# Kernel optimization log

Hardware: AMD Instinct MI355X
Metric: run time of the kernel (lower is better)

The kernel has to match this reference:

```python
import jax, jax.numpy as jnp
import numpy as np

H, D = 8, 16          # heads, per-head dim (hidden=128)
N_NEWS, N_INTER, F_IN, C_OUT = 30000, 60000, 768, 4
HID = H * D


def setup_inputs() -> dict:
    key = jax.random.key(0)
    ks = jax.random.split(key, 20)
    s = lambda i, shape, sc=0.05: (jax.random.normal(ks[i], shape, dtype=jnp.float32) * sc)
    inp = {
        "x_news": jax.random.normal(ks[0], (N_NEWS, F_IN), dtype=jnp.float32),
        "x_inter": jax.random.normal(ks[1], (N_INTER, F_IN), dtype=jnp.float32),
        "edge_nn": jax.random.randint(ks[2], (2, 480000), 0, N_NEWS),
        "edge_in": jax.random.randint(ks[3], (2, 960000), 0, N_NEWS),
        # per-node-type input projections (HANConv.proj)
        "W_news": s(4, (F_IN, HID)), "b_news": jnp.zeros((HID,), jnp.float32),
        "W_inter": s(5, (F_IN, HID)), "b_inter": jnp.zeros((HID,), jnp.float32),
        # per-edge-type node-level attention vectors (lin_src / lin_dst)
        "a_src_nn": s(6, (H, D), 0.2), "a_dst_nn": s(7, (H, D), 0.2),
        "a_src_in": s(8, (H, D), 0.2), "a_dst_in": s(9, (H, D), 0.2),
        # semantic-level attention (k_lin, q)
        "Wk": s(10, (HID, HID)), "bk": jnp.zeros((HID,), jnp.float32),
        "q": s(11, (HID,), 0.2),
        # output head
        "W_out": s(12, (HID, C_OUT)), "b_out": jnp.zeros((C_OUT,), jnp.float32),
    }
    return inp


def _han_conv(h_src, h_dst, edge, a_src, a_dst, n_dst):
    # node-level (GAT-style) attention for one edge type
    asrc = (h_src * a_src).sum(-1)            # [Ns, H]
    adst = (h_dst * a_dst).sum(-1)            # [Nd, H]
    src, dst = edge[0], edge[1]
    e = jax.nn.leaky_relu(asrc[src] + adst[dst], negative_slope=0.2)   # [E, H]
    m = jax.ops.segment_max(e, dst, num_segments=n_dst)                # [Nd, H]
    m = jnp.where(jnp.isfinite(m), m, jnp.float32(0))
    ex = jnp.exp(e - m[dst])
    denom = jax.ops.segment_sum(ex, dst, num_segments=n_dst)
    alpha = ex / (denom[dst] + jnp.float32(1e-16))                     # [E, H]
    out = jax.ops.segment_sum(h_src[src] * alpha[:, :, None], dst, num_segments=n_dst)
    return jax.nn.relu(out.reshape(n_dst, H * D))                      # [Nd, HID]


def reference(x_news, x_inter, edge_nn, edge_in,
              W_news, b_news, W_inter, b_inter,
              a_src_nn, a_dst_nn, a_src_in, a_dst_in,
              Wk, bk, q, W_out, b_out):
    # per-node-type projection, reshape to heads
    h_news = (x_news @ W_news + b_news).reshape(-1, H, D)
    h_inter = (x_inter @ W_inter + b_inter).reshape(-1, H, D)
    # per-edge-type node-level attention conv (dst is always 'news')
    out_nn = _han_conv(h_news, h_news, edge_nn, a_src_nn, a_dst_nn, N_NEWS)
    out_in = _han_conv(h_inter, h_news, edge_in, a_src_in, a_dst_in, N_NEWS)
    # semantic-level attention across metapaths
    outs = jnp.stack([out_nn, out_in])                       # [2, N, HID]
    score = (q * jnp.tanh(outs @ Wk + bk).mean(axis=1)).sum(-1)   # [2]
    beta = jax.nn.softmax(score, axis=0)
    fused = (beta[:, None, None] * outs).sum(0)              # [N, HID]
    # head: ELU + (eval-mode dropout = identity) + Linear
    return jax.nn.elu(fused) @ W_out + b_out
```

## Files before the change

kernel.cpp:

```cpp
#include <hip/hip_runtime.h>
#include <hip/hip_bf16.h>

#define N_NODES   30000
#define F_IN      768
#define HID       128
#define NHEAD     8
#define C_OUT     4

typedef short short8_t __attribute__((ext_vector_type(8)));
typedef float float4_t __attribute__((ext_vector_type(4)));
typedef int   int4_t   __attribute__((ext_vector_type(4)));

__device__ __forceinline__ float b2f(short u) {
    union { unsigned int i; float f; } v;
    v.i = ((unsigned int)(unsigned short)u) << 16;
    return v.f;
}
__device__ __forceinline__ short f2s(float f) {
    __hip_bfloat16 h = __float2bfloat16(f);
    short s; __builtin_memcpy(&s, &h, 2); return s;
}

#define OFF_H_NEWS      0UL
#define OFF_H_INTER     7680000UL
#define OFF_OUT_NN      15360000UL
#define OFF_OUT_IN      23040000UL
#define OFF_ASRC_NN     30720000UL
#define OFF_ADST_NN     31680000UL
#define OFF_ASRC_IN     32640000UL
#define OFF_ADST_IN     33600000UL
#define OFF_WT_NEWS     34560000UL
#define OFF_WT_INTER    34756608UL
#define OFF_RS_NN       34953216UL
#define OFF_RS_IN       35073280UL
#define OFF_SORT_NN     35193344UL
#define OFF_SORT_IN     37113344UL
#define OFF_ZERO        40953344UL
#define OFF_DEG_NN      40953344UL
#define OFF_FILL_NN     41073408UL
#define OFF_DEG_IN      41193472UL
#define OFF_FILL_IN     41313536UL
#define OFF_SSUM        41433600UL
#define OFF_CNT         41434624UL
#define ZERO_BYTES      481296UL
#define OFF_BETA        41434640UL
#define OFF_FLAG        41434648UL
#define OFF_CPAR        41434656UL
#define OFF_WKT         41470512UL

#define CP_B_NEWS  0
#define CP_B_INTER 128
#define CP_ASRC_NN 256
#define CP_ADST_NN 384
#define CP_ASRC_IN 512
#define CP_ADST_IN 640
#define CP_WK      768
#define CP_BK      17152
#define CP_Q       17280
#define CP_WOUT    17408
#define CP_BOUT    17920
#define CP_TOTAL   17924

#define PREP_CONV_BLOCKS 7
#define PREP_TW_BLOCKS   384
#define PREP_WK_BLOCKS   64
#define PREP_ZERO_BLOCKS 118
#define PREP_B0 PREP_CONV_BLOCKS
#define PREP_B1 (PREP_B0 + 2*PREP_TW_BLOCKS)
#define PREP_B2 (PREP_B1 + PREP_WK_BLOCKS)
#define PREP_TOTAL (PREP_B2 + PREP_ZERO_BLOCKS)

#define GEMM_BX 469

__global__ void detect_dtype(const unsigned int* __restrict__ x, int* __restrict__ flag) {
    __shared__ int cnt_s;
    if (threadIdx.x == 0) cnt_s = 0;
    __syncthreads();
    int sane = 0;
    for (int i = threadIdx.x; i < 16384; i += 1024) {
        unsigned int lo = x[i] & 0xFFFFu;
        unsigned int ex = (lo >> 7) & 0xFFu;
        if ((ex >= 107u && ex <= 147u) || lo == 0u || lo == 0x8000u) sane++;
    }
    atomicAdd(&cnt_s, sane);
    __syncthreads();
    if (threadIdx.x == 0) *flag = (cnt_s > 8192) ? 1 : 0;
}

struct SmallParams {
    const void* src[10];
    int n[10];
    int dstoff[10];
};

__global__ void prep(SmallParams sp, short* __restrict__ cp,
                     const void* __restrict__ Wn, const void* __restrict__ Wi,
                     const void* __restrict__ Wkraw,
                     short* __restrict__ WtN, short* __restrict__ WtI,
                     short* __restrict__ wkT,
                     char* __restrict__ zbase,
                     const int* __restrict__ flag) {
    const bool isbf = (*flag != 0);
    int b = blockIdx.x, tid = threadIdx.x;
    if (b < PREP_B0) {
        int idx = b * 256 + tid;
        for (int s = 0; s < 10; ++s) {
            if (idx < sp.n[s]) {
                short v = isbf ? ((const short*)sp.src[s])[idx]
                               : f2s(((const float*)sp.src[s])[idx]);
                cp[sp.dstoff[s] + idx] = v;
                return;
            }
            idx -= sp.n[s];
        }
    } else if (b < PREP_B1) {
        int bb = b - PREP_B0;
        int ty = bb >= PREP_TW_BLOCKS;
        const void* Wraw = ty ? Wi : Wn;
        short* Wt        = ty ? WtI : WtN;
        int idx = (bb - ty * PREP_TW_BLOCKS) * 256 + tid;
        if (idx < F_IN * HID) {
            int n = idx / F_IN;
            int k = idx - n * F_IN;
            Wt[idx] = isbf ? ((const short*)Wraw)[k * HID + n]
                           : f2s(((const float*)Wraw)[k * HID + n]);
        }
    } else if (b < PREP_B2) {
        int idx = (b - PREP_B1) * 256 + tid;
        if (idx < HID * HID) {
            int j = idx >> 7;
            int k = idx & 127;
            wkT[idx] = isbf ? ((const short*)Wkraw)[k * HID + j]
                            : f2s(((const float*)Wkraw)[k * HID + j]);
        }
    } else {
        size_t off = ((size_t)(b - PREP_B2) * 256 + tid) * 16;
        if (off < ZERO_BYTES) *(int4_t*)(zbase + off) = (int4_t){0, 0, 0, 0};
    }
}

#define BK   32
#define LDK  40

__global__ __launch_bounds__(256) void proj_count(
    const void* __restrict__ Xn, const void* __restrict__ Xi,
    const short* __restrict__ WtN, const short* __restrict__ WtI,
    const short* __restrict__ cp,
    short* __restrict__ Hn, short* __restrict__ Hi,
    float* __restrict__ asrc_nn, float* __restrict__ adst_nn,
    float* __restrict__ asrc_in, float* __restrict__ adst_in,
    const int* __restrict__ dnn, int Enn,
    const int* __restrict__ din, int Ein,
    int* __restrict__ deg_nn, int* __restrict__ deg_in,
    int M, const int* __restrict__ flag)
{
    __shared__ __align__(16) short As[64 * LDK];
    __shared__ __align__(16) short Bs[128 * LDK];

    int b = blockIdx.x;
    if (b >= 2 * GEMM_BX) {
        int i = (b - 2 * GEMM_BX) * 256 + threadIdx.x;
        if (i < Enn) {
            int d = dnn[i];
            if ((unsigned)d < (unsigned)N_NODES) atomicAdd(&deg_nn[d], 1);
        } else {
            int j = i - Enn;
            if (j < Ein) {
                int d = din[j];
                if ((unsigned)d < (unsigned)N_NODES) atomicAdd(&deg_in[d], 1);
            }
        }
        return;
    }

    const bool isbf = (*flag != 0);
    int ty = b >= GEMM_BX;
    int bx = b - ty * GEMM_BX;
    const void* Xraw = ty ? Xi : Xn;
    const short* Wt  = ty ? WtI : WtN;
    const short* bias = cp + (ty ? CP_B_INTER : CP_B_NEWS);
    short* Hout      = ty ? Hi : Hn;

    int m0   = bx * 64;
    int tid  = threadIdx.x;
    int lane = tid & 63;
    int wid  = tid >> 6;
    int quad = lane >> 4;
    int lm   = lane & 15;

    float4_t acc[8];
    #pragma unroll
    for (int c = 0; c < 8; ++c) acc[c] = (float4_t){0.f, 0.f, 0.f, 0.f};

    int sr  = tid >> 2;
    int skp = (tid & 3) * 8;

    for (int k0 = 0; k0 < F_IN; k0 += BK) {
        __syncthreads();
        {
            int gm = m0 + sr; if (gm >= M) gm = M - 1;
            short8_t av;
            if (isbf) {
                av = *(const short8_t*)((const short*)Xraw + (size_t)gm * F_IN + k0 + skp);
            } else {
                const float* xf = (const float*)Xraw + (size_t)gm * F_IN + k0 + skp;
                float4_t f0 = *(const float4_t*)xf;
                float4_t f1 = *(const float4_t*)(xf + 4);
                av[0] = f2s(f0[0]); av[1] = f2s(f0[1]); av[2] = f2s(f0[2]); av[3] = f2s(f0[3]);
                av[4] = f2s(f1[0]); av[5] = f2s(f1[1]); av[6] = f2s(f1[2]); av[7] = f2s(f1[3]);
            }
            *(short8_t*)(&As[sr * LDK + skp]) = av;
        }
        #pragma unroll
        for (int rep = 0; rep < 2; ++rep) {
            int r = sr + rep * 64;
            short8_t bv = *(const short8_t*)(Wt + (size_t)r * F_IN + k0 + skp);
            *(short8_t*)(&Bs[r * LDK + skp]) = bv;
        }
        __syncthreads();

        short8_t bfrag[8];
        #pragma unroll
        for (int c = 0; c < 8; ++c)
            bfrag[c] = *(const short8_t*)(&Bs[(c * 16 + lm) * LDK + quad * 8]);
        short8_t afrag = *(const short8_t*)(&As[(wid * 16 + lm) * LDK + quad * 8]);
        #pragma unroll
        for (int c = 0; c < 8; ++c)
            acc[c] = __builtin_amdgcn_mfma_f32_16x16x32_bf16(afrag, bfrag[c], acc[c], 0, 0, 0);
    }

    const short* aw0 = cp + (ty ? CP_ASRC_IN : CP_ASRC_NN);
    const short* aw1 = cp + CP_ADST_NN;
    const short* aw2 = cp + CP_ADST_IN;

    #pragma unroll
    for (int c = 0; c < 8; ++c) {
        int col = c * 16 + lm;
        float bv = b2f(bias[col]);
        float w0 = b2f(aw0[col]);
        float w1 = b2f(aw1[col]);
        float w2 = b2f(aw2[col]);
        #pragma unroll
        for (int r = 0; r < 4; ++r) {
            int gm = m0 + wid * 16 + quad * 4 + r;
            bool ok = gm < M;
            float hval = acc[c][r] + bv;
            if (ok) Hout[(size_t)gm * HID + col] = f2s(hval);
            if (ty == 0) {
                float d0 = hval * w0, d1 = hval * w1, d2 = hval * w2;
                #pragma unroll
                for (int off = 1; off < 16; off <<= 1) {
                    d0 += __shfl_xor(d0, off, 16);
                    d1 += __shfl_xor(d1, off, 16);
                    d2 += __shfl_xor(d2, off, 16);
                }
                if (lm == 0 && ok) {
                    asrc_nn[gm * NHEAD + c] = d0;
                    adst_nn[gm * NHEAD + c] = d1;
                    adst_in[gm * NHEAD + c] = d2;
                }
            } else {
                float d0 = hval * w0;
                #pragma unroll
                for (int off = 1; off < 16; off <<= 1)
                    d0 += __shfl_xor(d0, off, 16);
                if (lm == 0 && ok) asrc_in[gm * NHEAD + c] = d0;
            }
        }
    }
}

__global__ __launch_bounds__(256) void prefix_scan2(
    const int* __restrict__ deg_nn, int* __restrict__ rs_nn,
    const int* __restrict__ deg_in, int* __restrict__ rs_in, int n)
{
    const int* deg = blockIdx.x ? deg_in : deg_nn;
    int* row_start = blockIdx.x ? rs_in : rs_nn;
    __shared__ int psum[256];
    int tid = threadIdx.x;
    int chunk = (n + 255) / 256;
    int lo = tid * chunk;
    int hi = lo + chunk; if (hi > n) hi = n; if (lo > n) lo = n;
    int s = 0;
    for (int i = lo; i < hi; ++i) s += deg[i];
    psum[tid] = s;
    __syncthreads();
    for (int off = 1; off < 256; off <<= 1) {
        int v = (tid >= off) ? psum[tid - off] : 0;
        __syncthreads();
        psum[tid] += v;
        __syncthreads();
    }
    int base = tid ? psum[tid - 1] : 0;
    for (int i = lo; i < hi; ++i) { row_start[i] = base; base += deg[i]; }
    if (tid == 255) row_start[n] = psum[255];
}

__global__ void scatter_edges2(const int* __restrict__ enn, int Enn,
                               const int* __restrict__ ein, int Ein,
                               const int* __restrict__ rs_nn, int* __restrict__ fill_nn,
                               int* __restrict__ sort_nn,
                               const int* __restrict__ rs_in, int* __restrict__ fill_in,
                               int* __restrict__ sort_in) {
    int i = blockIdx.x * 256 + threadIdx.x;
    if (i < Enn) {
        int d = enn[Enn + i];
        if (d >= 0 && d < N_NODES) {
            int pos = rs_nn[d] + atomicAdd(&fill_nn[d], 1);
            if (pos >= 0 && pos < Enn) sort_nn[pos] = enn[i];
        }
    } else {
        int j = i - Enn;
        if (j < Ein) {
            int d = ein[Ein + j];
            if (d >= 0 && d < N_NODES) {
                int pos = rs_in[d] + atomicAdd(&fill_in[d], 1);
                if (pos >= 0 && pos < Ein) sort_in[pos] = ein[j];
            }
        }
    }
}

__global__ __launch_bounds__(256) void aggregate2(
    const short* __restrict__ Hnn, const short* __restrict__ Hin,
    const float* __restrict__ asrc_nn, const float* __restrict__ adst_nn,
    const float* __restrict__ asrc_in, const float* __restrict__ adst_in,
    const int* __restrict__ rs_nn, const int* __restrict__ rs_in,
    const int* __restrict__ sort_nn, const int* __restrict__ sort_in,
    short* __restrict__ out_nn, short* __restrict__ out_in)
{
    int tid = threadIdx.x, w = tid >> 6, lane = tid & 63;
    int type = blockIdx.y;
    const short* H    = type ? Hin : Hnn;
    const float* asrc = type ? asrc_in : asrc_nn;
    const float* adst = type ? adst_in : adst_nn;
    const int*   rs   = type ? rs_in : rs_nn;
    const int*   ss   = type ? sort_in : sort_nn;
    short* outb       = type ? out_in : out_nn;

    int dn = blockIdx.x * 4 + w;
    int start = rs[dn], end = rs[dn + 1];
    int head = lane >> 3;
    float adv = adst[dn * NHEAD + head];
    const short* Hl = H + lane * 2;

    float den = 0.f, a0 = 0.f, a1 = 0.f;
    for (int base = start; base < end; base += 64) {
        int nb = end - base; if (nb > 64) nb = 64;
        int myidx = 0;
        if (base + lane < end) {
            int t = ss[base + lane];
            myidx = (t < 0) ? 0 : (t >= N_NODES ? N_NODES - 1 : t);
        }
        int j = 0;
        for (; j + 2 <= nb; j += 2) {
            int s0 = __shfl(myidx, j, 64);
            int s1 = __shfl(myidx, j + 1, 64);
            float v0 = asrc[s0 * NHEAD + head];
            float v1 = asrc[s1 * NHEAD + head];
            unsigned int q0 = *(const unsigned int*)(Hl + (size_t)s0 * HID);
            unsigned int q1 = *(const unsigned int*)(Hl + (size_t)s1 * HID);
            float e0 = v0 + adv, e1 = v1 + adv;
            e0 = fmaxf(e0, 0.2f * e0); e1 = fmaxf(e1, 0.2f * e1);
            e0 = fminf(e0, 80.f);      e1 = fminf(e1, 80.f);
            float x0 = __expf(e0), x1 = __expf(e1);
            union { unsigned int u; float f; } cl0, ch0, cl1, ch1;
            cl0.u = q0 << 16; ch0.u = q0 & 0xFFFF0000u;
            cl1.u = q1 << 16; ch1.u = q1 & 0xFFFF0000u;
            den += x0; den += x1;
            a0 = fmaf(x0, cl0.f, a0); a0 = fmaf(x1, cl1.f, a0);
            a1 = fmaf(x0, ch0.f, a1); a1 = fmaf(x1, ch1.f, a1);
        }
        if (j < nb) {
            int s0 = __shfl(myidx, j, 64);
            float v0 = asrc[s0 * NHEAD + head];
            unsigned int q0 = *(const unsigned int*)(Hl + (size_t)s0 * HID);
            float e0 = v0 + adv;
            e0 = fmaxf(e0, 0.2f * e0);
            e0 = fminf(e0, 80.f);
            float x0 = __expf(e0);
            union { unsigned int u; float f; } cl0, ch0;
            cl0.u = q0 << 16; ch0.u = q0 & 0xFFFF0000u;
            den += x0;
            a0 = fmaf(x0, cl0.f, a0);
            a1 = fmaf(x0, ch0.f, a1);
        }
    }
    float inv = 1.f / (den + 1e-16f);
    unsigned int lo16 = (unsigned short)f2s(fmaxf(a0 * inv, 0.f));
    unsigned int hi16 = (unsigned short)f2s(fmaxf(a1 * inv, 0.f));
    *(unsigned int*)(outb + (size_t)dn * HID + lane * 2) = lo16 | (hi16 << 16);
}

__global__ __launch_bounds__(256) void score_mfma(
    const short* __restrict__ out_nn, const short* __restrict__ out_in,
    const short* __restrict__ wkT, const short* __restrict__ cp,
    float* __restrict__ Ssum, int* __restrict__ done_cnt,
    float* __restrict__ beta, int total_blocks)
{
    __shared__ float col_s[HID];
    __shared__ int lastflag;
    int tid  = threadIdx.x;
    int lane = tid & 63;
    int wid  = tid >> 6;
    int quad = lane >> 4;
    int lm   = lane & 15;
    const short* src = blockIdx.y ? out_in : out_nn;
    int m0 = blockIdx.x * 128;

    if (tid < HID) col_s[tid] = 0.f;
    __syncthreads();

    float4_t acc[2][8];
    #pragma unroll
    for (int i = 0; i < 2; ++i)
        #pragma unroll
        for (int c = 0; c < 8; ++c)
            acc[i][c] = (float4_t){0.f, 0.f, 0.f, 0.f};

    #pragma unroll
    for (int kc = 0; kc < 4; ++kc) {
        short8_t bfrag[8];
        #pragma unroll
        for (int c = 0; c < 8; ++c)
            bfrag[c] = *(const short8_t*)(wkT + (c * 16 + lm) * HID + kc * 32 + quad * 8);
        #pragma unroll
        for (int i = 0; i < 2; ++i) {
            int gm = m0 + wid * 32 + i * 16 + lm;
            if (gm >= N_NODES) gm = N_NODES - 1;
            short8_t afrag = *(const short8_t*)(src + (size_t)gm * HID + kc * 32 + quad * 8);
            #pragma unroll
            for (int c = 0; c < 8; ++c)
                acc[i][c] = __builtin_amdgcn_mfma_f32_16x16x32_bf16(afrag, bfrag[c], acc[i][c], 0, 0, 0);
        }
    }

    #pragma unroll
    for (int c = 0; c < 8; ++c) {
        int col = c * 16 + lm;
        float bkc = b2f(cp[CP_BK + col]);
        float lsum = 0.f;
        #pragma unroll
        for (int i = 0; i < 2; ++i)
            #pragma unroll
            for (int r = 0; r < 4; ++r) {
                int node = m0 + wid * 32 + i * 16 + quad * 4 + r;
                if (node < N_NODES) {
                    float a = acc[i][c][r] + bkc;
                    a = fminf(fmaxf(a, -15.f), 15.f);
                    float t = __expf(2.f * a);
                    lsum += (t - 1.f) / (t + 1.f);
                }
            }
        float v = lsum;
        v += __shfl_down(v, 32, 64);
        v += __shfl_down(v, 16, 64);
        if (quad == 0) atomicAdd(&col_s[col], v);
    }
    __syncthreads();
    if (tid < HID) atomicAdd(&Ssum[blockIdx.y * HID + tid], col_s[tid]);
    __syncthreads();

    if (tid == 0) {
        __threadfence();
        int old = atomicAdd(done_cnt, 1);
        lastflag = (old == total_blocks - 1) ? 1 : 0;
    }
    __syncthreads();
    if (lastflag && tid < 64) {
        float s00 = atomicAdd(&Ssum[tid], 0.f);
        float s01 = atomicAdd(&Ssum[tid + 64], 0.f);
        float s10 = atomicAdd(&Ssum[128 + tid], 0.f);
        float s11 = atomicAdd(&Ssum[192 + tid], 0.f);
        float q0 = b2f(cp[CP_Q + tid]), q1 = b2f(cp[CP_Q + tid + 64]);
        float v0 = q0 * s00 + q1 * s01;
        float v1 = q0 * s10 + q1 * s11;
        #pragma unroll
        for (int off = 32; off; off >>= 1) {
            v0 += __shfl_down(v0, off, 64);
            v1 += __shfl_down(v1, off, 64);
        }
        if (tid == 0) {
            float sc0 = v0 / (float)N_NODES;
            float sc1 = v1 / (float)N_NODES;
            float mx = fmaxf(sc0, sc1);
            float e0 = __expf(sc0 - mx), e1 = __expf(sc1 - mx);
            float inv = 1.f / (e0 + e1);
            beta[0] = e0 * inv;
            beta[1] = e1 * inv;
        }
    }
}

__global__ __launch_bounds__(256) void final_out(
    const short* __restrict__ out_nn, const short* __restrict__ out_in,
    const float* __restrict__ beta, const short* __restrict__ cp,
    void* __restrict__ Yraw, const int* __restrict__ flag)
{
    bool isbf = (*flag != 0);
    int tid = threadIdx.x, lane = tid & 63, w = tid >> 6;
    int n = blockIdx.x * 4 + w;
    float b0 = beta[0], b1 = beta[1];
    unsigned int u0 = *(const unsigned int*)(out_nn + (size_t)n * HID + lane * 2);
    unsigned int u1 = *(const unsigned int*)(out_in + (size_t)n * HID + lane * 2);
    union { unsigned int u; float f; } t;
    t.u = u0 << 16;          float f0 = b0 * t.f;
    t.u = u0 & 0xFFFF0000u;  float f1 = b0 * t.f;
    t.u = u1 << 16;          f0 += b1 * t.f;
    t.u = u1 & 0xFFFF0000u;  f1 += b1 * t.f;
    float e0 = (f0 > 0.f) ? f0 : expm1f(f0);
    float e1 = (f1 > 0.f) ? f1 : expm1f(f1);
    int c0 = lane * 2, c1 = lane * 2 + 1;
    float p[C_OUT];
    #pragma unroll
    for (int c = 0; c < C_OUT; ++c)
        p[c] = e0 * b2f(cp[CP_WOUT + c0 * C_OUT + c]) + e1 * b2f(cp[CP_WOUT + c1 * C_OUT + c]);
    #pragma unroll
    for (int off = 32; off; off >>= 1)
        #pragma unroll
        for (int c = 0; c < C_OUT; ++c) p[c] += __shfl_down(p[c], off, 64);
    if (lane == 0) {
        #pragma unroll
        for (int c = 0; c < C_OUT; ++c) {
            float r = p[c] + b2f(cp[CP_BOUT + c]);
            if (isbf) ((__hip_bfloat16*)Yraw)[n * C_OUT + c] = __float2bfloat16(r);
            else      ((float*)Yraw)[n * C_OUT + c] = r;
        }
    }
}

extern "C" void kernel_launch(void* const* d_in, const int* in_sizes, int n_in,
                              void* d_out, int out_size, void* d_ws, size_t ws_size,
                              hipStream_t stream) {
    const void* x_news  = d_in[0];
    const void* x_inter = d_in[1];
    const int*  edge_nn = (const int*)d_in[2];
    const int*  edge_in = (const int*)d_in[3];

    int E_nn = in_sizes[2] / 2;
    int E_in = in_sizes[3] / 2;

    char* ws = (char*)d_ws;
    short* h_news  = (short*)(ws + OFF_H_NEWS);
    short* h_inter = (short*)(ws + OFF_H_INTER);
    short* out_nn  = (short*)(ws + OFF_OUT_NN);
    short* out_in  = (short*)(ws + OFF_OUT_IN);
    float* asrc_nn = (float*)(ws + OFF_ASRC_NN);
    float* adst_nn = (float*)(ws + OFF_ADST_NN);
    float* asrc_in = (float*)(ws + OFF_ASRC_IN);
    float* adst_in = (float*)(ws + OFF_ADST_IN);
    short* wt_news  = (short*)(ws + OFF_WT_NEWS);
    short* wt_inter = (short*)(ws + OFF_WT_INTER);
    int* rs_nn   = (int*)(ws + OFF_RS_NN);
    int* rs_in   = (int*)(ws + OFF_RS_IN);
    int* sort_nn = (int*)(ws + OFF_SORT_NN);
    int* sort_in = (int*)(ws + OFF_SORT_IN);
    int* deg_nn  = (int*)(ws + OFF_DEG_NN);
    int* fill_nn = (int*)(ws + OFF_FILL_NN);
    int* deg_in  = (int*)(ws + OFF_DEG_IN);
    int* fill_in = (int*)(ws + OFF_FILL_IN);
    float* Ssum  = (float*)(ws + OFF_SSUM);
    int*   dcnt  = (int*)(ws + OFF_CNT);
    float* beta  = (float*)(ws + OFF_BETA);
    int*   flag  = (int*)(ws + OFF_FLAG);
    short* cp    = (short*)(ws + OFF_CPAR);
    short* wkT   = (short*)(ws + OFF_WKT);

    detect_dtype<<<1, 1024, 0, stream>>>((const unsigned int*)x_news, flag);

    SmallParams sp;
    const int srcidx[10] = {5, 7, 8, 9, 10, 11, 13, 14, 15, 16};
    const int ns[10]     = {128, 128, 128, 128, 128, 128, 128, 128, 512, 4};
    const int doff[10]   = {CP_B_NEWS, CP_B_INTER, CP_ASRC_NN, CP_ADST_NN, CP_ASRC_IN,
                            CP_ADST_IN, CP_BK, CP_Q, CP_WOUT, CP_BOUT};
    for (int i = 0; i < 10; ++i) { sp.src[i] = d_in[srcidx[i]]; sp.n[i] = ns[i]; sp.dstoff[i] = doff[i]; }

    prep<<<PREP_TOTAL, 256, 0, stream>>>(sp, cp, d_in[4], d_in[6], d_in[12],
                                         wt_news, wt_inter, wkT, ws + OFF_ZERO, flag);

    int cnt_blocks = (E_nn + E_in + 255) / 256;
    proj_count<<<2 * GEMM_BX + cnt_blocks, 256, 0, stream>>>(
        x_news, x_inter, wt_news, wt_inter, cp, h_news, h_inter,
        asrc_nn, adst_nn, asrc_in, adst_in,
        edge_nn + E_nn, E_nn, edge_in + E_in, E_in, deg_nn, deg_in,
        N_NODES, flag);

    prefix_scan2<<<2, 256, 0, stream>>>(deg_nn, rs_nn, deg_in, rs_in, N_NODES);

    scatter_edges2<<<cnt_blocks, 256, 0, stream>>>(
        edge_nn, E_nn, edge_in, E_in, rs_nn, fill_nn, sort_nn, rs_in, fill_in, sort_in);

    aggregate2<<<dim3(N_NODES / 4, 2), 256, 0, stream>>>(
        h_news, h_inter, asrc_nn, adst_nn, asrc_in, adst_in,
        rs_nn, rs_in, sort_nn, sort_in, out_nn, out_in);

    int score_bx = (N_NODES + 127) / 128;
    score_mfma<<<dim3(score_bx, 2), 256, 0, stream>>>(
        out_nn, out_in, wkT, cp, Ssum, dcnt, beta, 2 * score_bx);

    final_out<<<N_NODES / 4, 256, 0, stream>>>(out_nn, out_in, beta, cp, d_out, flag);
}
```

Before: 584.9 us.

## Rewrite projection GEMM to load operands directly into registers with prefetch

```diff
diff --git a/kernel.cpp b/kernel.cpp
--- a/kernel.cpp
+++ b/kernel.cpp
@@ -54,7 +54,6 @@
 #define CP_ADST_NN 384
 #define CP_ASRC_IN 512
 #define CP_ADST_IN 640
-#define CP_WK      768
 #define CP_BK      17152
 #define CP_Q       17280
 #define CP_WOUT    17408
@@ -70,7 +69,7 @@
 #define PREP_B2 (PREP_B1 + PREP_WK_BLOCKS)
 #define PREP_TOTAL (PREP_B2 + PREP_ZERO_BLOCKS)
 
-#define GEMM_BX 469
+#define GEMM_BX 235
 
 __global__ void detect_dtype(const unsigned int* __restrict__ x, int* __restrict__ flag) {
     __shared__ int cnt_s;
@@ -139,8 +138,166 @@
     }
 }
 
-#define BK   32
-#define LDK  40
+template<bool ISBF>
+__device__ __forceinline__ void gemm_body(
+    const void* __restrict__ Xraw, const short* __restrict__ Wt,
+    const short* __restrict__ cp, short* __restrict__ Hout,
+    float* __restrict__ dot0, float* __restrict__ dot1, float* __restrict__ dot2,
+    int ty, int m0, int M, short* __restrict__ ep_all)
+{
+    int tid  = threadIdx.x;
+    int lane = tid & 63;
+    int wid  = tid >> 6;
+    int quad = lane >> 4;
+    int lm   = lane & 15;
+
+    const short* bias = cp + (ty ? CP_B_INTER : CP_B_NEWS);
+    const short* aw0  = cp + (ty ? CP_ASRC_IN : CP_ASRC_NN);
+    const short* aw1  = cp + CP_ADST_NN;
+    const short* aw2  = cp + CP_ADST_IN;
+
+    int gr[2];
+    #pragma unroll
+    for (int i = 0; i < 2; ++i) {
+        int gm = m0 + wid * 32 + i * 16 + lm;
+        gr[i] = gm < M ? gm : M - 1;
+    }
+
+    const float* af[2];
+    const short* as[2];
+    if (ISBF) {
+        as[0] = (const short*)Xraw + (size_t)gr[0] * F_IN + quad * 8;
+        as[1] = (const short*)Xraw + (size_t)gr[1] * F_IN + quad * 8;
+    } else {
+        af[0] = (const float*)Xraw + (size_t)gr[0] * F_IN + quad * 8;
+        af[1] = (const float*)Xraw + (size_t)gr[1] * F_IN + quad * 8;
+    }
+    const short* bbase = Wt + (size_t)lm * F_IN + quad * 8;
+
+    float4_t acc[2][8];
+    #pragma unroll
+    for (int i = 0; i < 2; ++i)
+        #pragma unroll
+        for (int c = 0; c < 8; ++c)
+            acc[i][c] = (float4_t){0.f, 0.f, 0.f, 0.f};
+
+    short8_t bN[8];
+    short8_t aNs[2];
+    float4_t aNf[2][2];
+    #pragma unroll
+    for (int c = 0; c < 8; ++c)
+        bN[c] = *(const short8_t*)(bbase + (size_t)c * 16 * F_IN);
+    if (ISBF) {
+        aNs[0] = *(const short8_t*)as[0];
+        aNs[1] = *(const short8_t*)as[1];
+    } else {
+        aNf[0][0] = *(const float4_t*)af[0]; aNf[0][1] = *(const float4_t*)(af[0] + 4);
+        aNf[1][0] = *(const float4_t*)af[1]; aNf[1][1] = *(const float4_t*)(af[1] + 4);
+    }
+
+    #pragma unroll 2
+    for (int kc = 0; kc < 24; ++kc) {
+        short8_t bC[8];
+        short8_t aCs[2];
+        float4_t aCf[2][2];
+        #pragma unroll
+        for (int c = 0; c < 8; ++c) bC[c] = bN[c];
+        if (ISBF) { aCs[0] = aNs[0]; aCs[1] = aNs[1]; }
+        else {
+            aCf[0][0] = aNf[0][0]; aCf[0][1] = aNf[0][1];
+            aCf[1][0] = aNf[1][0]; aCf[1][1] = aNf[1][1];
+        }
+
+        if (kc < 23) {
+            int k1 = (kc + 1) * 32;
+            #pragma unroll
+            for (int c = 0; c < 8; ++c)
+                bN[c] = *(const short8_t*)(bbase + (size_t)c * 16 * F_IN + k1);
+            if (ISBF) {
+                aNs[0] = *(const short8_t*)(as[0] + k1);
+                aNs[1] = *(const short8_t*)(as[1] + k1);
+            } else {
+                aNf[0][0] = *(const float4_t*)(af[0] + k1);
+                aNf[0][1] = *(const float4_t*)(af[0] + k1 + 4);
+                aNf[1][0] = *(const float4_t*)(af[1] + k1);
+                aNf[1][1] = *(const float4_t*)(af[1] + k1 + 4);
+            }
+        }
+
+        short8_t afr[2];
+        if (ISBF) { afr[0] = aCs[0]; afr[1] = aCs[1]; }
+        else {
+            #pragma unroll
+            for (int i = 0; i < 2; ++i)
+                #pragma unroll
+                for (int j = 0; j < 4; ++j) {
+                    afr[i][j]     = f2s(aCf[i][0][j]);
+                    afr[i][4 + j] = f2s(aCf[i][1][j]);
+                }
+        }
+
+        #pragma unroll
+        for (int c = 0; c < 8; ++c)
+            #pragma unroll
+            for (int i = 0; i < 2; ++i)
+                acc[i][c] = __builtin_amdgcn_mfma_f32_16x16x32_bf16(afr[i], bC[c], acc[i][c], 0, 0, 0);
+    }
+
+    short* ep = ep_all + wid * (32 * 130);
+
+    #pragma unroll
+    for (int i = 0; i < 2; ++i)
+        #pragma unroll
+        for (int r = 0; r < 4; ++r) {
+            int lrow = i * 16 + quad * 4 + r;
+            int gm = m0 + wid * 32 + lrow;
+            bool ok = gm < M;
+            float d0a[8], d1a[8], d2a[8];
+            #pragma unroll
+            for (int c = 0; c < 8; ++c) {
+                int col = c * 16 + lm;
+                float hval = acc[i][c][r] + b2f(bias[col]);
+                ep[lrow * 130 + col] = f2s(hval);
+                float d0 = hval * b2f(aw0[col]);
+                float d1 = hval * b2f(aw1[col]);
+                float d2 = hval * b2f(aw2[col]);
+                #pragma unroll
+                for (int off = 1; off < 16; off <<= 1) {
+                    d0 += __shfl_xor(d0, off, 16);
+                    if (ty == 0) {
+                        d1 += __shfl_xor(d1, off, 16);
+                        d2 += __shfl_xor(d2, off, 16);
+                    }
+                }
+                d0a[c] = d0; d1a[c] = d1; d2a[c] = d2;
+            }
+            if (lm == 0 && ok) {
+                float4_t v0 = {d0a[0], d0a[1], d0a[2], d0a[3]};
+                float4_t v1 = {d0a[4], d0a[5], d0a[6], d0a[7]};
+                *(float4_t*)(dot0 + (size_t)gm * NHEAD)     = v0;
+                *(float4_t*)(dot0 + (size_t)gm * NHEAD + 4) = v1;
+                if (ty == 0) {
+                    float4_t w0 = {d1a[0], d1a[1], d1a[2], d1a[3]};
+                    float4_t w1 = {d1a[4], d1a[5], d1a[6], d1a[7]};
+                    *(float4_t*)(dot1 + (size_t)gm * NHEAD)     = w0;
+                    *(float4_t*)(dot1 + (size_t)gm * NHEAD + 4) = w1;
+                    float4_t u0 = {d2a[0], d2a[1], d2a[2], d2a[3]};
+                    float4_t u1 = {d2a[4], d2a[5], d2a[6], d2a[7]};
+                    *(float4_t*)(dot2 + (size_t)gm * NHEAD)     = u0;
+                    *(float4_t*)(dot2 + (size_t)gm * NHEAD + 4) = u1;
+                }
+            }
+        }
+    __syncthreads();
+    #pragma unroll
+    for (int j = 0; j < 8; ++j) {
+        int row = j * 4 + (lane >> 4);
+        short8_t v = *(const short8_t*)(&ep_all[wid * (32 * 130) + row * 130 + (lane & 15) * 8]);
+        int gm = m0 + wid * 32 + row;
+        if (gm < M)
+            *(short8_t*)(&Hout[(size_t)gm * HID + (lane & 15) * 8]) = v;
+    }
+}
 
 __global__ __launch_bounds__(256) void proj_count(
     const void* __restrict__ Xn, const void* __restrict__ Xi,
@@ -154,8 +311,7 @@
     int* __restrict__ deg_nn, int* __restrict__ deg_in,
     int M, const int* __restrict__ flag)
 {
-    __shared__ __align__(16) short As[64 * LDK];
-    __shared__ __align__(16) short Bs[128 * LDK];
+    __shared__ __align__(16) short Ep[4 * 32 * 130];
 
     int b = blockIdx.x;
     if (b >= 2 * GEMM_BX) {
@@ -176,98 +332,15 @@
     const bool isbf = (*flag != 0);
     int ty = b >= GEMM_BX;
     int bx = b - ty * GEMM_BX;
+    int m0 = bx * 128;
+
     const void* Xraw = ty ? Xi : Xn;
     const short* Wt  = ty ? WtI : WtN;
-    const short* bias = cp + (ty ? CP_B_INTER : CP_B_NEWS);
     short* Hout      = ty ? Hi : Hn;
-
-    int m0   = bx * 64;
-    int tid  = threadIdx.x;
-    int lane = tid & 63;
-    int wid  = tid >> 6;
-    int quad = lane >> 4;
-    int lm   = lane & 15;
-
-    float4_t acc[8];
-    #pragma unroll
-    for (int c = 0; c < 8; ++c) acc[c] = (float4_t){0.f, 0.f, 0.f, 0.f};
-
-    int sr  = tid >> 2;
-    int skp = (tid & 3) * 8;
-
-    for (int k0 = 0; k0 < F_IN; k0 += BK) {
-        __syncthreads();
-        {
-            int gm = m0 + sr; if (gm >= M) gm = M - 1;
-            short8_t av;
-            if (isbf) {
-                av = *(const short8_t*)((const short*)Xraw + (size_t)gm * F_IN + k0 + skp);
-            } else {
-                const float* xf = (const float*)Xraw + (size_t)gm * F_IN + k0 + skp;
-                float4_t f0 = *(const float4_t*)xf;
-                float4_t f1 = *(const float4_t*)(xf + 4);
-                av[0] = f2s(f0[0]); av[1] = f2s(f0[1]); av[2] = f2s(f0[2]); av[3] = f2s(f0[3]);
-                av[4] = f2s(f1[0]); av[5] = f2s(f1[1]); av[6] = f2s(f1[2]); av[7] = f2s(f1[3]);
-            }
-            *(short8_t*)(&As[sr * LDK + skp]) = av;
-        }
-        #pragma unroll
-        for (int rep = 0; rep < 2; ++rep) {
-            int r = sr + rep * 64;
-            short8_t bv = *(const short8_t*)(Wt + (size_t)r * F_IN + k0 + skp);
-            *(short8_t*)(&Bs[r * LDK + skp]) = bv;
-        }
-        __syncthreads();
-
-        short8_t bfrag[8];
-        #pragma unroll
-        for (int c = 0; c < 8; ++c)
-            bfrag[c] = *(const short8_t*)(&Bs[(c * 16 + lm) * LDK + quad * 8]);
-        short8_t afrag = *(const short8_t*)(&As[(wid * 16 + lm) * LDK + quad * 8]);
-        #pragma unroll
-        for (int c = 0; c < 8; ++c)
-            acc[c] = __builtin_amdgcn_mfma_f32_16x16x32_bf16(afrag, bfrag[c], acc[c], 0, 0, 0);
-    }
-
-    const short* aw0 = cp + (ty ? CP_ASRC_IN : CP_ASRC_NN);
-    const short* aw1 = cp + CP_ADST_NN;
-    const short* aw2 = cp + CP_ADST_IN;
-
-    #pragma unroll
-    for (int c = 0; c < 8; ++c) {
-        int col = c * 16 + lm;
-        float bv = b2f(bias[col]);
-        float w0 = b2f(aw0[col]);
-        float w1 = b2f(aw1[col]);
-        float w2 = b2f(aw2[col]);
-        #pragma unroll
-        for (int r = 0; r < 4; ++r) {
-            int gm = m0 + wid * 16 + quad * 4 + r;
-            bool ok = gm < M;
-            float hval = acc[c][r] + bv;
-            if (ok) Hout[(size_t)gm * HID + col] = f2s(hval);
-            if (ty == 0) {
-                float d0 = hval * w0, d1 = hval * w1, d2 = hval * w2;
-                #pragma unroll
-                for (int off = 1; off < 16; off <<= 1) {
-                    d0 += __shfl_xor(d0, off, 16);
-                    d1 += __shfl_xor(d1, off, 16);
-                    d2 += __shfl_xor(d2, off, 16);
-                }
-                if (lm == 0 && ok) {
-                    asrc_nn[gm * NHEAD + c] = d0;
-                    adst_nn[gm * NHEAD + c] = d1;
-                    adst_in[gm * NHEAD + c] = d2;
-                }
-            } else {
-                float d0 = hval * w0;
-                #pragma unroll
-                for (int off = 1; off < 16; off <<= 1)
-                    d0 += __shfl_xor(d0, off, 16);
-                if (lm == 0 && ok) asrc_in[gm * NHEAD + c] = d0;
-            }
-        }
-    }
+    float* dot0      = ty ? asrc_in : asrc_nn;
+
+    if (isbf) gemm_body<true >(Xraw, Wt, cp, Hout, dot0, adst_nn, adst_in, ty, m0, M, Ep);
+    else      gemm_body<false>(Xraw, Wt, cp, Hout, dot0, adst_nn, adst_in, ty, m0, M, Ep);
 }
 
 __global__ __launch_bounds__(256) void prefix_scan2(
```

After: 627.4 us. 1.07x slower.

## Double-buffer projection GEMM with register prefetch and LDS-staged epilogue

Applied to the files above, without the earlier changes.

```diff
diff --git a/kernel.cpp b/kernel.cpp
--- a/kernel.cpp
+++ b/kernel.cpp
@@ -54,7 +54,6 @@
 #define CP_ADST_NN 384
 #define CP_ASRC_IN 512
 #define CP_ADST_IN 640
-#define CP_WK      768
 #define CP_BK      17152
 #define CP_Q       17280
 #define CP_WOUT    17408
@@ -71,6 +70,9 @@
 #define PREP_TOTAL (PREP_B2 + PREP_ZERO_BLOCKS)
 
 #define GEMM_BX 469
+#define LDK     40
+#define ABUF    2560
+#define BUFSZ   7680
 
 __global__ void detect_dtype(const unsigned int* __restrict__ x, int* __restrict__ flag) {
     __shared__ int cnt_s;
@@ -139,8 +141,141 @@
     }
 }
 
-#define BK   32
-#define LDK  40
+template<bool ISBF>
+__device__ __forceinline__ void gemm_body(
+    const void* __restrict__ Xraw, const short* __restrict__ Wt,
+    const short* __restrict__ cp, short* __restrict__ Hout,
+    float* __restrict__ dot0, float* __restrict__ dot1, float* __restrict__ dot2,
+    int ty, int m0, int M, short* __restrict__ SB)
+{
+    int tid  = threadIdx.x;
+    int lane = tid & 63;
+    int wid  = tid >> 6;
+    int quad = lane >> 4;
+    int lm   = lane & 15;
+    int sr   = tid >> 2;
+    int skp  = (tid & 3) * 8;
+
+    int ga = m0 + sr; if (ga >= M) ga = M - 1;
+    const short* asrc_s = (const short*)Xraw + (size_t)ga * F_IN + skp;
+    const float* asrc_f = (const float*)Xraw + (size_t)ga * F_IN + skp;
+    const short* bsrc0  = Wt + (size_t)sr * F_IN + skp;
+    const short* bsrc1  = Wt + (size_t)(sr + 64) * F_IN + skp;
+
+    short8_t avr;
+    float4_t af0, af1;
+    short8_t bvr0, bvr1;
+
+    auto LOAD = [&](int k0) {
+        if (ISBF) {
+            avr = *(const short8_t*)(asrc_s + k0);
+        } else {
+            af0 = *(const float4_t*)(asrc_f + k0);
+            af1 = *(const float4_t*)(asrc_f + k0 + 4);
+        }
+        bvr0 = *(const short8_t*)(bsrc0 + k0);
+        bvr1 = *(const short8_t*)(bsrc1 + k0);
+    };
+    auto STORE = [&](short* buf) {
+        short8_t av;
+        if (ISBF) av = avr;
+        else {
+            #pragma unroll
+            for (int j = 0; j < 4; ++j) {
+                av[j]     = f2s(af0[j]);
+                av[4 + j] = f2s(af1[j]);
+            }
+        }
+        *(short8_t*)(buf + sr * LDK + skp)                = av;
+        *(short8_t*)(buf + ABUF + sr * LDK + skp)         = bvr0;
+        *(short8_t*)(buf + ABUF + (sr + 64) * LDK + skp)  = bvr1;
+    };
+
+    float4_t acc[8];
+    #pragma unroll
+    for (int c = 0; c < 8; ++c) acc[c] = (float4_t){0.f, 0.f, 0.f, 0.f};
+
+    LOAD(0);
+    STORE(SB);
+    LOAD(32);
+    __syncthreads();
+
+    for (int kc = 0; kc < 24; ++kc) {
+        short* buf = SB + (kc & 1) * BUFSZ;
+        short* nxt = SB + ((kc & 1) ^ 1) * BUFSZ;
+
+        short8_t bfrag[8];
+        #pragma unroll
+        for (int c = 0; c < 8; ++c)
+            bfrag[c] = *(const short8_t*)(buf + ABUF + (c * 16 + lm) * LDK + quad * 8);
+        short8_t afrag = *(const short8_t*)(buf + (wid * 16 + lm) * LDK + quad * 8);
+
+        if (kc < 23) STORE(nxt);
+        if (kc < 22) LOAD((kc + 2) * 32);
+
+        #pragma unroll
+        for (int c = 0; c < 8; ++c)
+            acc[c] = __builtin_amdgcn_mfma_f32_16x16x32_bf16(afrag, bfrag[c], acc[c], 0, 0, 0);
+        __syncthreads();
+    }
+
+    const short* bias = cp + (ty ? CP_B_INTER : CP_B_NEWS);
+    const short* aw0  = cp + (ty ? CP_ASRC_IN : CP_ASRC_NN);
+    const short* aw1  = cp + CP_ADST_NN;
+    const short* aw2  = cp + CP_ADST_IN;
+
+    short* ep = SB;
+
+    #pragma unroll
+    for (int r = 0; r < 4; ++r) {
+        int erow = wid * 16 + quad * 4 + r;
+        int gm = m0 + erow;
+        bool ok = gm < M;
+        float d0a[8], d1a[8], d2a[8];
+        #pragma unroll
+        for (int c = 0; c < 8; ++c) {
+            int col = c * 16 + lm;
+            float hval = acc[c][r] + b2f(bias[col]);
+            ep[erow * 130 + col] = f2s(hval);
+            float d0 = hval * b2f(aw0[col]);
+            float d1 = hval * b2f(aw1[col]);
+            float d2 = hval * b2f(aw2[col]);
+            #pragma unroll
+            for (int off = 1; off < 16; off <<= 1) {
+                d0 += __shfl_xor(d0, off, 16);
+                if (ty == 0) {
+                    d1 += __shfl_xor(d1, off, 16);
+                    d2 += __shfl_xor(d2, off, 16);
+                }
+            }
+            d0a[c] = d0; d1a[c] = d1; d2a[c] = d2;
+        }
+        if (lm == 0 && ok) {
+            float4_t v0 = {d0a[0], d0a[1], d0a[2], d0a[3]};
+            float4_t v1 = {d0a[4], d0a[5], d0a[6], d0a[7]};
+            *(float4_t*)(dot0 + (size_t)gm * NHEAD)     = v0;
+            *(float4_t*)(dot0 + (size_t)gm * NHEAD + 4) = v1;
+            if (ty == 0) {
+                float4_t w0 = {d1a[0], d1a[1], d1a[2], d1a[3]};
+                float4_t w1 = {d1a[4], d1a[5], d1a[6], d1a[7]};
+                *(float4_t*)(dot1 + (size_t)gm * NHEAD)     = w0;
+                *(float4_t*)(dot1 + (size_t)gm * NHEAD + 4) = w1;
+                float4_t u0 = {d2a[0], d2a[1], d2a[2], d2a[3]};
+                float4_t u1 = {d2a[4], d2a[5], d2a[6], d2a[7]};
+                *(float4_t*)(dot2 + (size_t)gm * NHEAD)     = u0;
+                *(float4_t*)(dot2 + (size_t)gm * NHEAD + 4) = u1;
+            }
+        }
+    }
+    #pragma unroll
+    for (int j = 0; j < 4; ++j) {
+        int erow = wid * 16 + j * 4 + quad;
+        int gm = m0 + erow;
+        short8_t v = *(const short8_t*)(&ep[erow * 130 + lm * 8]);
+        if (gm < M)
+            *(short8_t*)(&Hout[(size_t)gm * HID + lm * 8]) = v;
+    }
+}
 
 __global__ __launch_bounds__(256) void proj_count(
     const void* __restrict__ Xn, const void* __restrict__ Xi,
@@ -154,8 +289,7 @@
     int* __restrict__ deg_nn, int* __restrict__ deg_in,
     int M, const int* __restrict__ flag)
 {
-    __shared__ __align__(16) short As[64 * LDK];
-    __shared__ __align__(16) short Bs[128 * LDK];
+    __shared__ __align__(16) short SB[2 * BUFSZ];
 
     int b = blockIdx.x;
     if (b >= 2 * GEMM_BX) {
@@ -176,98 +310,15 @@
     const bool isbf = (*flag != 0);
     int ty = b >= GEMM_BX;
     int bx = b - ty * GEMM_BX;
+    int m0 = bx * 64;
+
     const void* Xraw = ty ? Xi : Xn;
     const short* Wt  = ty ? WtI : WtN;
-    const short* bias = cp + (ty ? CP_B_INTER : CP_B_NEWS);
     short* Hout      = ty ? Hi : Hn;
-
-    int m0   = bx * 64;
-    int tid  = threadIdx.x;
-    int lane = tid & 63;
-    int wid  = tid >> 6;
-    int quad = lane >> 4;
-    int lm   = lane & 15;
-
-    float4_t acc[8];
-    #pragma unroll
-    for (int c = 0; c < 8; ++c) acc[c] = (float4_t){0.f, 0.f, 0.f, 0.f};
-
-    int sr  = tid >> 2;
-    int skp = (tid & 3) * 8;
-
-    for (int k0 = 0; k0 < F_IN; k0 += BK) {
-        __syncthreads();
-        {
-            int gm = m0 + sr; if (gm >= M) gm = M - 1;
-            short8_t av;
-            if (isbf) {
-                av = *(const short8_t*)((const short*)Xraw + (size_t)gm * F_IN + k0 + skp);
-            } else {
-                const float* xf = (const float*)Xraw + (size_t)gm * F_IN + k0 + skp;
-                float4_t f0 = *(const float4_t*)xf;
-                float4_t f1 = *(const float4_t*)(xf + 4);
-                av[0] = f2s(f0[0]); av[1] = f2s(f0[1]); av[2] = f2s(f0[2]); av[3] = f2s(f0[3]);
-                av[4] = f2s(f1[0]); av[5] = f2s(f1[1]); av[6] = f2s(f1[2]); av[7] = f2s(f1[3]);
-            }
-            *(short8_t*)(&As[sr * LDK + skp]) = av;
-        }
-        #pragma unroll
-        for (int rep = 0; rep < 2; ++rep) {
-            int r = sr + rep * 64;
-            short8_t bv = *(const short8_t*)(Wt + (size_t)r * F_IN + k0 + skp);
-            *(short8_t*)(&Bs[r * LDK + skp]) = bv;
-        }
-        __syncthreads();
-
-        short8_t bfrag[8];
-        #pragma unroll
-        for (int c = 0; c < 8; ++c)
-            bfrag[c] = *(const short8_t*)(&Bs[(c * 16 + lm) * LDK + quad * 8]);
-        short8_t afrag = *(const short8_t*)(&As[(wid * 16 + lm) * LDK + quad * 8]);
-        #pragma unroll
-        for (int c = 0; c < 8; ++c)
-            acc[c] = __builtin_amdgcn_mfma_f32_16x16x32_bf16(afrag, bfrag[c], acc[c], 0, 0, 0);
-    }
-
-    const short* aw0 = cp + (ty ? CP_ASRC_IN : CP_ASRC_NN);
-    const short* aw1 = cp + CP_ADST_NN;
-    const short* aw2 = cp + CP_ADST_IN;
-
-    #pragma unroll
-    for (int c = 0; c < 8; ++c) {
-        int col = c * 16 + lm;
-        float bv = b2f(bias[col]);
-        float w0 = b2f(aw0[col]);
-        float w1 = b2f(aw1[col]);
-        float w2 = b2f(aw2[col]);
-        #pragma unroll
-        for (int r = 0; r < 4; ++r) {
-            int gm = m0 + wid * 16 + quad * 4 + r;
-            bool ok = gm < M;
-            float hval = acc[c][r] + bv;
-            if (ok) Hout[(size_t)gm * HID + col] = f2s(hval);
-            if (ty == 0) {
-                float d0 = hval * w0, d1 = hval * w1, d2 = hval * w2;
-                #pragma unroll
-                for (int off = 1; off < 16; off <<= 1) {
-                    d0 += __shfl_xor(d0, off, 16);
-                    d1 += __shfl_xor(d1, off, 16);
-                    d2 += __shfl_xor(d2, off, 16);
-                }
-                if (lm == 0 && ok) {
-                    asrc_nn[gm * NHEAD + c] = d0;
-                    adst_nn[gm * NHEAD + c] = d1;
-                    adst_in[gm * NHEAD + c] = d2;
-                }
-            } else {
-                float d0 = hval * w0;
-                #pragma unroll
-                for (int off = 1; off < 16; off <<= 1)
-                    d0 += __shfl_xor(d0, off, 16);
-                if (lm == 0 && ok) asrc_in[gm * NHEAD + c] = d0;
-            }
-        }
-    }
+    float* dot0      = ty ? asrc_in : asrc_nn;
+
+    if (isbf) gemm_body<true >(Xraw, Wt, cp, Hout, dot0, adst_nn, adst_in, ty, m0, M, SB);
+    else      gemm_body<false>(Xraw, Wt, cp, Hout, dot0, adst_nn, adst_in, ty, m0, M, SB);
 }
 
 __global__ __launch_bounds__(256) void prefix_scan2(
```

New measurement: 622.4 us. 1.06x slower.
